# Optimization experiments

Hardware: AMD Instinct MI355X
Metric: run time of the kernel (lower is better)

The kernel has to match this reference:

```python
import jax, jax.numpy as jnp
import numpy as np

# Module dims (match init_kwargs / input_specs)
V = 25        # number of graph nodes (chain skeleton)
K = 3         # max receptive-field size (neighbors incl. self), padded
CIN = 64
COUT = 64
N = 16
T = 512
TK = 3        # temporal_kernel
PAD = TK // 2 # time_pad default


def _build_graph():
    # Chain adjacency with self-links: node i <-> {i-1, i, i+1}
    A = np.zeros((V, V), np.float32)
    for i in range(V):
        A[i, i] = 1.0
        if i > 0:
            A[i, i - 1] = 1.0
        if i < V - 1:
            A[i, i + 1] = 1.0
    # Pad each node's neighbor list to K entries; mask marks real neighbors.
    idx = np.zeros((V, K), np.int32)
    mask = np.zeros((V, K), bool)
    for i in range(V):
        nb = np.where(A[i] != 0)[0]
        idx[i, : len(nb)] = nb
        mask[i, : len(nb)] = True
    return idx, mask


def setup_inputs() -> dict:
    key = jax.random.key(0)
    k_x, k_w, k_b = jax.random.split(key, 3)
    x = jax.random.normal(k_x, (N, CIN, V, T), dtype=jnp.float32)
    # One Conv2d kernel per node: [V, C_out, C_in, K, TK]; padded neighbor
    # slots are zeroed via mask inside reference().
    W = jax.random.normal(k_w, (V, COUT, CIN, K, TK), dtype=jnp.float32) * 0.05
    b = jax.random.normal(k_b, (V, COUT), dtype=jnp.float32) * 0.05
    idx_np, mask_np = _build_graph()
    return {
        "x": x,
        "W": W,
        "b": b,
        "idx": jnp.asarray(idx_np),
        "mask": jnp.asarray(mask_np),
    }


def reference(x, W, b, idx, mask):
    # x: [N, C, V, T]; W: [V, O, C, K, TK]; b: [V, O]; idx/mask: [V, K]
    Tt = x.shape[-1]
    # Zero out padded neighbor slots so padded rows contribute nothing
    # (equivalent to torch's variable-height per-node kernels).
    Wm = jnp.where(mask[:, None, None, :, None], W, 0.0)
    # Temporal zero padding (Conv2d padding=(0, time_pad))
    xp = jnp.pad(x, ((0, 0), (0, 0), (0, 0), (PAD, PAD)))
    # Batched neighbor gather: [N, C, V, K, T + 2*PAD]
    g = xp[:, :, idx, :]
    # Cross-correlation over the TK temporal taps (stride 1)
    out = jnp.zeros((x.shape[0], W.shape[1], V, Tt), dtype=x.dtype)
    for kt in range(TK):
        out = out + jnp.einsum(
            "ncvkt,vock->novt", g[..., kt : kt + Tt], Wm[..., kt]
        )
    out = out + b.T[None, :, :, None]  # per-node bias [O, V]
    return out
```

## Files before the change

kernel.cpp:

```cpp
#include <hip/hip_runtime.h>
#include <hip/hip_bf16.h>

#define NB   16
#define CINC 64
#define COUTC 64
#define NV   25
#define TLEN 512
#define KK   3
#define TKK  3

typedef short short8 __attribute__((ext_vector_type(8)));
typedef float f32x4  __attribute__((ext_vector_type(4)));
typedef float f32x16 __attribute__((ext_vector_type(16)));

#define XT_ROWS 514
#define XS_BYTES 16640
#define NWT3BLK (NV * 9)

__device__ __forceinline__ unsigned pack_bf16(float lo, float hi) {
  __hip_bfloat16 l = __float2bfloat16(lo);
  __hip_bfloat16 h = __float2bfloat16(hi);
  unsigned short ul = *reinterpret_cast<unsigned short*>(&l);
  unsigned short uh = *reinterpret_cast<unsigned short*>(&h);
  return (unsigned)ul | ((unsigned)uh << 16);
}

__global__ __launch_bounds__(256) void prep_all(
    const float* __restrict__ x, const float* __restrict__ W,
    const unsigned char* __restrict__ mask_raw,
    __hip_bfloat16* __restrict__ Wt3, __hip_bfloat16* __restrict__ xT) {
  __shared__ float ts[64][65];
  int bid = blockIdx.x;
  if (bid < NWT3BLK) {
    int blk = bid;
    int v = blk / 9, kkt = blk % 9, k = kkt / 3, kt = kkt % 3;
    const int* mi = (const int*)mask_raw;
    int ok = 1;
    for (int i = 0; i < 18; ++i) {
      int m = mi[i];
      if (m != 0 && m != 1) ok = 0;
    }
    int m = ok ? mi[v * KK + k] : (int)(mask_raw[v * KK + k] != 0);
    const float* Wv = W + (size_t)v * COUTC * CINC * 9;
    __hip_bfloat16* dst = Wt3 + (size_t)blk * 4096;
    for (int i = threadIdx.x; i < 4096; i += 256) {
      int e     = i & 7;
      int lane  = (i >> 3) & 63;
      int ks    = (i >> 9) & 3;
      int oslab = i >> 11;
      int o = oslab * 32 + (lane & 31);
      int c = ks * 16 + 8 * (lane >> 5) + e;
      float val = m ? Wv[(o * CINC + c) * 9 + k * 3 + kt] : 0.f;
      dst[i] = __float2bfloat16(val);
    }
    return;
  }
  bid -= NWT3BLK;
  const int tb = (bid & 7) * 64;
  const int vn = bid >> 3;
  const int v  = vn % NV;
  const int n  = vn / NV;
  const int tid = threadIdx.x;
  for (int i = tid; i < 1024; i += 256) {
    int c = i >> 4, tq = (i & 15) * 4;
    float4 val = *(const float4*)(x + (((size_t)n * CINC + c) * NV + v) * TLEN + tb + tq);
    ts[c][tq + 0] = val.x;
    ts[c][tq + 1] = val.y;
    ts[c][tq + 2] = val.z;
    ts[c][tq + 3] = val.w;
  }
  __syncthreads();
  unsigned* base = (unsigned*)(xT + ((size_t)(n * NV + v) * XT_ROWS) * CINC);
  for (int i = tid; i < 2048; i += 256) {
    int c2 = i & 31, t = i >> 5;
    base[(tb + 1 + t) * 32 + c2] = pack_bf16(ts[2 * c2][t], ts[2 * c2 + 1][t]);
  }
  if (tb == 0 && tid < 32) base[tid] = 0u;
  if (tb == TLEN - 64 && tid < 32) base[513 * 32 + tid] = 0u;
}

__device__ __forceinline__ const char* slab_base(const __hip_bfloat16* xT,
                                                 int n, int vk, int tb) {
  return (const char*)xT + ((size_t)(n * NV + vk) * XT_ROWS + tb) * 128;
}

__device__ __forceinline__ void stage_slab(const char* gbase, char* lbase,
                                           int wave, int lane) {
  for (int c = wave; c < 17; c += 4) {
    int L = c * 1024 + lane * 16;
    if (L < XS_BYTES) {
      int g = L ^ (((L >> 7) & 7) << 4);
      __builtin_amdgcn_global_load_lds(
          (const __attribute__((address_space(1))) void*)(gbase + g),
          (__attribute__((address_space(3))) void*)(lbase + c * 1024),
          16, 0, 0);
    }
  }
}

__global__ __launch_bounds__(256, 2) void lcn_mfma32(
    const __hip_bfloat16* __restrict__ xT,
    const __hip_bfloat16* __restrict__ Wt3,
    const float* __restrict__ bias,
    const int* __restrict__ idx,
    float* __restrict__ out) {
  __shared__ char xs[2][2][XS_BYTES];

  const int tb   = blockIdx.x * 128;
  const int np   = blockIdx.y;
  const int v    = blockIdx.z;
  const int n0   = np * 2;
  const int tid  = threadIdx.x;
  const int lane = tid & 63;
  const int wave = tid >> 6;
  const int wt   = wave * 32;
  const int hi   = lane >> 5;
  const int l31  = lane & 31;

  f32x16 acc00 = {}, acc01 = {};
  f32x16 acc10 = {}, acc11 = {};

  {
    const int vk0 = idx[v * KK + 0];
    stage_slab(slab_base(xT, n0, vk0, tb),     xs[0][0], wave, lane);
    stage_slab(slab_base(xT, n0 + 1, vk0, tb), xs[0][1], wave, lane);
  }

  const short8* wbase = (const short8*)Wt3;

  for (int k = 0; k < KK; ++k) {
    __syncthreads();

    if (k < KK - 1) {
      const int vk1 = idx[v * KK + k + 1];
      char* nbuf0 = xs[(k + 1) & 1][0];
      char* nbuf1 = xs[(k + 1) & 1][1];
      stage_slab(slab_base(xT, n0, vk1, tb),     nbuf0, wave, lane);
      stage_slab(slab_base(xT, n0 + 1, vk1, tb), nbuf1, wave, lane);
    }

    const char* cb0 = xs[k & 1][0];
    const char* cb1 = xs[k & 1][1];
    const int blk0 = (v * KK + k) * TKK;

#pragma unroll
    for (int kt = 0; kt < TKK; ++kt) {
      short8 a0[4], a1[4];
      {
        const short8* p0 = wbase + (((blk0 + kt) * 2 + 0) << 8) + lane;
        const short8* p1 = wbase + (((blk0 + kt) * 2 + 1) << 8) + lane;
#pragma unroll
        for (int ks = 0; ks < 4; ++ks) {
          a0[ks] = p0[ks << 6];
          a1[ks] = p1[ks << 6];
        }
      }
      const int r  = wt + l31 + kt;
      const int sw = (r & 7) << 4;
      const int co = hi * 16;
      const char* bp0 = cb0 + r * 128;
      const char* bp1 = cb1 + r * 128;
#pragma unroll
      for (int ks = 0; ks < 4; ++ks) {
        short8 bfr = *(const short8*)(bp0 + ((co + 32 * ks) ^ sw));
        acc00 = __builtin_amdgcn_mfma_f32_32x32x16_bf16(a0[ks], bfr, acc00, 0, 0, 0);
        acc01 = __builtin_amdgcn_mfma_f32_32x32x16_bf16(a1[ks], bfr, acc01, 0, 0, 0);
      }
#pragma unroll
      for (int ks = 0; ks < 4; ++ks) {
        short8 bfr = *(const short8*)(bp1 + ((co + 32 * ks) ^ sw));
        acc10 = __builtin_amdgcn_mfma_f32_32x32x16_bf16(a0[ks], bfr, acc10, 0, 0, 0);
        acc11 = __builtin_amdgcn_mfma_f32_32x32x16_bf16(a1[ks], bfr, acc11, 0, 0, 0);
      }
    }
  }

  const float* bv = bias + v * COUTC;
  const int t = tb + wt + l31;
#pragma unroll
  for (int nn = 0; nn < 2; ++nn) {
#pragma unroll
    for (int os = 0; os < 2; ++os) {
      const f32x16& acc = nn ? (os ? acc11 : acc10) : (os ? acc01 : acc00);
#pragma unroll
      for (int reg = 0; reg < 16; ++reg) {
        int o = os * 32 + 4 * hi + (reg & 3) + 8 * (reg >> 2);
        out[(((size_t)(n0 + nn) * COUTC + o) * NV + v) * TLEN + t] =
            acc[reg] + bv[o];
      }
    }
  }
}

__global__ void prep_mask_kernel(const int* __restrict__ mask_raw,
                                 int* __restrict__ mask_out) {
  __shared__ int fmt;
  if (threadIdx.x == 0) {
    int ok = 1;
    for (int i = 0; i < 18; ++i) {
      int m = mask_raw[i];
      if (m != 0 && m != 1) ok = 0;
    }
    fmt = ok;
  }
  __syncthreads();
  int i = threadIdx.x;
  if (i < NV * KK) {
    int m;
    if (fmt) m = mask_raw[i];
    else     m = (((const unsigned char*)mask_raw)[i] != 0) ? 1 : 0;
    mask_out[i] = m;
  }
}

__global__ void prep_wt_kernel(const float* __restrict__ W,
                               float* __restrict__ Wt) {
  int v   = blockIdx.x / 9;
  int kkt = blockIdx.x % 9;
  const float* Wv = W + (size_t)v * COUTC * CINC * 9;
  float* dst = Wt + (size_t)blockIdx.x * (CINC * COUTC);
  for (int i = threadIdx.x; i < CINC * COUTC; i += 256) {
    int c = i >> 6;
    int o = i & 63;
    dst[i] = Wv[(o * CINC + c) * 9 + kkt];
  }
}

__global__ __launch_bounds__(256, 4) void lcn_main(
    const float* __restrict__ x, const float* __restrict__ Wt,
    const float* __restrict__ b, const int* __restrict__ idx,
    const int* __restrict__ maskn, float* __restrict__ out) {
  __shared__ float xsf[CINC][66];
  __shared__ float wsh[CINC][COUTC];
  const int tb  = blockIdx.x * 64;
  const int v   = blockIdx.y;
  const int n   = blockIdx.z;
  const int tid = threadIdx.x;
  const int t0  = tid & 63;
  const int og  = tid >> 6;
  float acc[16];
#pragma unroll
  for (int j = 0; j < 16; ++j) acc[j] = 0.f;
  for (int k = 0; k < KK; ++k) {
    const int vk = idx[v * KK + k];
    const int mk = maskn[v * KK + k];
    __syncthreads();
    for (int i = tid; i < CINC * 66; i += 256) {
      int c  = i / 66;
      int tt = i - c * 66;
      int gt = tb - 1 + tt;
      float val = 0.f;
      if (mk && gt >= 0 && gt < TLEN)
        val = x[(((size_t)n * CINC + c) * NV + vk) * TLEN + gt];
      xsf[c][tt] = val;
    }
    for (int kt = 0; kt < TKK; ++kt) {
      __syncthreads();
      const float4* src =
          (const float4*)(Wt + ((size_t)(v * KK + k) * TKK + kt) * (CINC * COUTC));
      for (int i = tid; i < CINC * COUTC / 4; i += 256)
        ((float4*)wsh)[i] = src[i];
      __syncthreads();
#pragma unroll 4
      for (int c = 0; c < CINC; ++c) {
        float xv = xsf[c][t0 + kt];
        const float4* wrow = (const float4*)&wsh[c][og * 16];
#pragma unroll
        for (int j4 = 0; j4 < 4; ++j4) {
          float4 wv = wrow[j4];
          acc[j4 * 4 + 0] = fmaf(wv.x, xv, acc[j4 * 4 + 0]);
          acc[j4 * 4 + 1] = fmaf(wv.y, xv, acc[j4 * 4 + 1]);
          acc[j4 * 4 + 2] = fmaf(wv.z, xv, acc[j4 * 4 + 2]);
          acc[j4 * 4 + 3] = fmaf(wv.w, xv, acc[j4 * 4 + 3]);
        }
      }
    }
  }
#pragma unroll
  for (int j = 0; j < 16; ++j) {
    int o = og * 16 + j;
    out[(((size_t)n * COUTC + o) * NV + v) * TLEN + tb + t0] =
        acc[j] + b[v * COUTC + o];
  }
}

extern "C" void kernel_launch(void* const* d_in, const int* in_sizes, int n_in,
                              void* d_out, int out_size, void* d_ws, size_t ws_size,
                              hipStream_t stream) {
  const float* x    = (const float*)d_in[0];
  const float* W    = (const float*)d_in[1];
  const float* b    = (const float*)d_in[2];
  const int*   idx  = (const int*)d_in[3];
  const void*  mask = (const void*)d_in[4];
  float* out = (float*)d_out;

  const size_t WT3_BYTES = (size_t)NV * 9 * 4096 * sizeof(__hip_bfloat16);
  const size_t XT_BYTES  = (size_t)NB * NV * XT_ROWS * CINC * sizeof(__hip_bfloat16);
  const size_t NEED      = 512 + WT3_BYTES + XT_BYTES + 2048;

  if (ws_size >= NEED) {
    __hip_bfloat16* Wt3 = (__hip_bfloat16*)((char*)d_ws + 512);
    __hip_bfloat16* xT  = (__hip_bfloat16*)((char*)d_ws + 512 + WT3_BYTES);
    hipLaunchKernelGGL(prep_all, dim3(NWT3BLK + 8 * NV * NB), dim3(256), 0,
                       stream, x, W, (const unsigned char*)mask, Wt3, xT);
    hipLaunchKernelGGL(lcn_mfma32, dim3(TLEN / 128, NB / 2, NV), dim3(256), 0,
                       stream, xT, Wt3, b, idx, out);
  } else {
    int*   maskn = (int*)d_ws;
    float* Wt    = (float*)((char*)d_ws + 512);
    hipLaunchKernelGGL(prep_mask_kernel, dim3(1), dim3(128), 0, stream,
                       (const int*)mask, maskn);
    hipLaunchKernelGGL(prep_wt_kernel, dim3(NV * KK * TKK), dim3(256), 0, stream,
                       W, Wt);
    hipLaunchKernelGGL(lcn_main, dim3(TLEN / 64, NV, NB), dim3(256), 0, stream,
                       x, Wt, b, idx, maskn, out);
  }
}
```

Before: 54.13 us.

## Process one batch per block and stage all neighbor slabs upfront

Each block now handles a single batch element instead of two, doubling the grid, and loads all three neighbor slabs into LDS at once before one barrier, replacing the double-buffered per-neighbor pipeline. Accumulators drop from four to two, which lowers register pressure. The occupancy hint of two blocks per CU is removed. In exchange, weight fragments are reloaded from global memory twice as often, since they are no longer shared across two batches, and staging no longer overlaps with compute.

```diff
diff --git a/kernel.cpp b/kernel.cpp
--- a/kernel.cpp
+++ b/kernel.cpp
@@ -84,32 +84,17 @@
   return (const char*)xT + ((size_t)(n * NV + vk) * XT_ROWS + tb) * 128;
 }
 
-__device__ __forceinline__ void stage_slab(const char* gbase, char* lbase,
-                                           int wave, int lane) {
-  for (int c = wave; c < 17; c += 4) {
-    int L = c * 1024 + lane * 16;
-    if (L < XS_BYTES) {
-      int g = L ^ (((L >> 7) & 7) << 4);
-      __builtin_amdgcn_global_load_lds(
-          (const __attribute__((address_space(1))) void*)(gbase + g),
-          (__attribute__((address_space(3))) void*)(lbase + c * 1024),
-          16, 0, 0);
-    }
-  }
-}
-
-__global__ __launch_bounds__(256, 2) void lcn_mfma32(
+__global__ __launch_bounds__(256) void lcn_mfma32(
     const __hip_bfloat16* __restrict__ xT,
     const __hip_bfloat16* __restrict__ Wt3,
     const float* __restrict__ bias,
     const int* __restrict__ idx,
     float* __restrict__ out) {
-  __shared__ char xs[2][2][XS_BYTES];
+  __shared__ char xs[KK][XS_BYTES];
 
   const int tb   = blockIdx.x * 128;
-  const int np   = blockIdx.y;
+  const int n    = blockIdx.y;
   const int v    = blockIdx.z;
-  const int n0   = np * 2;
   const int tid  = threadIdx.x;
   const int lane = tid & 63;
   const int wave = tid >> 6;
@@ -117,32 +102,32 @@
   const int hi   = lane >> 5;
   const int l31  = lane & 31;
 
-  f32x16 acc00 = {}, acc01 = {};
-  f32x16 acc10 = {}, acc11 = {};
-
   {
-    const int vk0 = idx[v * KK + 0];
-    stage_slab(slab_base(xT, n0, vk0, tb),     xs[0][0], wave, lane);
-    stage_slab(slab_base(xT, n0 + 1, vk0, tb), xs[0][1], wave, lane);
-  }
-
+    const char* g0 = slab_base(xT, n, idx[v * KK + 0], tb);
+    const char* g1 = slab_base(xT, n, idx[v * KK + 1], tb);
+    const char* g2 = slab_base(xT, n, idx[v * KK + 2], tb);
+    for (int j = wave; j < 3 * 17; j += 4) {
+      int slab = j / 17, c = j % 17;
+      const char* gb = slab == 0 ? g0 : (slab == 1 ? g1 : g2);
+      int L = c * 1024 + lane * 16;
+      if (L < XS_BYTES) {
+        int g = L ^ (((L >> 7) & 7) << 4);
+        __builtin_amdgcn_global_load_lds(
+            (const __attribute__((address_space(1))) void*)(gb + g),
+            (__attribute__((address_space(3))) void*)(&xs[slab][c * 1024]),
+            16, 0, 0);
+      }
+    }
+  }
+  __syncthreads();
+
+  f32x16 acc0 = {}, acc1 = {};
   const short8* wbase = (const short8*)Wt3;
 
+#pragma unroll
   for (int k = 0; k < KK; ++k) {
-    __syncthreads();
-
-    if (k < KK - 1) {
-      const int vk1 = idx[v * KK + k + 1];
-      char* nbuf0 = xs[(k + 1) & 1][0];
-      char* nbuf1 = xs[(k + 1) & 1][1];
-      stage_slab(slab_base(xT, n0, vk1, tb),     nbuf0, wave, lane);
-      stage_slab(slab_base(xT, n0 + 1, vk1, tb), nbuf1, wave, lane);
-    }
-
-    const char* cb0 = xs[k & 1][0];
-    const char* cb1 = xs[k & 1][1];
+    const char* cb = xs[k];
     const int blk0 = (v * KK + k) * TKK;
-
 #pragma unroll
     for (int kt = 0; kt < TKK; ++kt) {
       short8 a0[4], a1[4];
@@ -158,19 +143,12 @@
       const int r  = wt + l31 + kt;
       const int sw = (r & 7) << 4;
       const int co = hi * 16;
-      const char* bp0 = cb0 + r * 128;
-      const char* bp1 = cb1 + r * 128;
+      const char* bp = cb + r * 128;
 #pragma unroll
       for (int ks = 0; ks < 4; ++ks) {
-        short8 bfr = *(const short8*)(bp0 + ((co + 32 * ks) ^ sw));
-        acc00 = __builtin_amdgcn_mfma_f32_32x32x16_bf16(a0[ks], bfr, acc00, 0, 0, 0);
-        acc01 = __builtin_amdgcn_mfma_f32_32x32x16_bf16(a1[ks], bfr, acc01, 0, 0, 0);
-      }
-#pragma unroll
-      for (int ks = 0; ks < 4; ++ks) {
-        short8 bfr = *(const short8*)(bp1 + ((co + 32 * ks) ^ sw));
-        acc10 = __builtin_amdgcn_mfma_f32_32x32x16_bf16(a0[ks], bfr, acc10, 0, 0, 0);
-        acc11 = __builtin_amdgcn_mfma_f32_32x32x16_bf16(a1[ks], bfr, acc11, 0, 0, 0);
+        short8 bfr = *(const short8*)(bp + ((co + 32 * ks) ^ sw));
+        acc0 = __builtin_amdgcn_mfma_f32_32x32x16_bf16(a0[ks], bfr, acc0, 0, 0, 0);
+        acc1 = __builtin_amdgcn_mfma_f32_32x32x16_bf16(a1[ks], bfr, acc1, 0, 0, 0);
       }
     }
   }
@@ -178,16 +156,12 @@
   const float* bv = bias + v * COUTC;
   const int t = tb + wt + l31;
 #pragma unroll
-  for (int nn = 0; nn < 2; ++nn) {
-#pragma unroll
-    for (int os = 0; os < 2; ++os) {
-      const f32x16& acc = nn ? (os ? acc11 : acc10) : (os ? acc01 : acc00);
-#pragma unroll
-      for (int reg = 0; reg < 16; ++reg) {
-        int o = os * 32 + 4 * hi + (reg & 3) + 8 * (reg >> 2);
-        out[(((size_t)(n0 + nn) * COUTC + o) * NV + v) * TLEN + t] =
-            acc[reg] + bv[o];
-      }
+  for (int os = 0; os < 2; ++os) {
+    const f32x16& acc = os ? acc1 : acc0;
+#pragma unroll
+    for (int reg = 0; reg < 16; ++reg) {
+      int o = os * 32 + 4 * hi + (reg & 3) + 8 * (reg >> 2);
+      out[(((size_t)n * COUTC + o) * NV + v) * TLEN + t] = acc[reg] + bv[o];
     }
   }
 }
@@ -303,7 +277,7 @@
     __hip_bfloat16* xT  = (__hip_bfloat16*)((char*)d_ws + 512 + WT3_BYTES);
     hipLaunchKernelGGL(prep_all, dim3(NWT3BLK + 8 * NV * NB), dim3(256), 0,
                        stream, x, W, (const unsigned char*)mask, Wt3, xT);
-    hipLaunchKernelGGL(lcn_mfma32, dim3(TLEN / 128, NB / 2, NV), dim3(256), 0,
+    hipLaunchKernelGGL(lcn_mfma32, dim3(TLEN / 128, NB, NV), dim3(256), 0,
                        stream, xT, Wt3, b, idx, out);
   } else {
     int*   maskn = (int*)d_ws;
```

New measurement: 54.59 us. Within noise of the previous version (+0.8%).
